# Performance work log

Measured on AMD Instinct MI355X. Metric: run time of the kernel, lower is better.

The kernel has to match this reference:

```python
import jax, jax.numpy as jnp
import numpy as np

HIDDEN = 256
HEADS = 1
HEAD_DIM = HIDDEN // HEADS  # internal_dim == hidden (downsample_rate=1)
SQ = 4096        # 64x64 current-frame tokens
N_MEM = 4        # memory frames
N_OBJ = 64       # object-pointer tokens excluded from RoPE
SK = N_MEM * SQ + N_OBJ  # 16448


def _rotate_pairwise(x):
    # [x0, x1, x2, x3, ...] -> [-x1, x0, -x3, x2, ...]
    s = x.shape
    x = x.reshape(s[:-1] + (s[-1] // 2, 2))
    return jnp.stack([-x[..., 1], x[..., 0]], axis=-1).reshape(s)


def setup_inputs() -> dict:
    key = jax.random.key(0)
    ks = jax.random.split(key, 16)
    d = {}
    d["query"] = jax.random.normal(ks[0], (1, 1, SQ, HIDDEN), jnp.float32)
    d["key"] = jax.random.normal(ks[1], (1, 1, SK, HIDDEN), jnp.float32)
    d["value"] = jax.random.normal(ks[2], (1, 1, SK, HIDDEN), jnp.float32)
    # rotary tables broadcast over (B*P, heads) like in the keras code
    d["cos"] = jax.random.uniform(ks[3], (1, 1, SQ, HEAD_DIM), jnp.float32, -1.0, 1.0)
    d["sin"] = jax.random.uniform(ks[4], (1, 1, SQ, HEAD_DIM), jnp.float32, -1.0, 1.0)
    w = 0.02
    d["q_w"] = jax.random.normal(ks[5], (HIDDEN, HIDDEN), jnp.float32) * w
    d["q_b"] = jnp.zeros((HIDDEN,), jnp.float32)
    d["k_w"] = jax.random.normal(ks[6], (HIDDEN, HIDDEN), jnp.float32) * w
    d["k_b"] = jnp.zeros((HIDDEN,), jnp.float32)
    d["v_w"] = jax.random.normal(ks[7], (HIDDEN, HIDDEN), jnp.float32) * w
    d["v_b"] = jnp.zeros((HIDDEN,), jnp.float32)
    d["o_w"] = jax.random.normal(ks[8], (HIDDEN, HIDDEN), jnp.float32) * w
    d["o_b"] = jnp.zeros((HIDDEN,), jnp.float32)
    d["num_k_exclude_rope"] = N_OBJ
    return d


def reference(query, key, value, cos, sin, q_w, q_b, k_w, k_b, v_w, v_b, o_w, o_b, num_k_exclude_rope):
    B, P, Sq, _ = query.shape
    Sk = key.shape[2]
    nex = int(num_k_exclude_rope)

    def heads(x):  # (B,P,S,internal) -> (B*P, H, S, hd)
        s = x.shape
        return x.reshape(s[0] * s[1], s[2], HEADS, HEAD_DIM).transpose(0, 2, 1, 3)

    q = heads(query @ q_w + q_b)
    k = heads(key @ k_w + k_b)
    v = heads(value @ v_w + v_b)

    # 2D rotary embedding (fp32 math, as in the original)
    qf = q.astype(jnp.float32)
    q_emb = (qf * cos + _rotate_pairwise(qf) * sin).astype(q.dtype)

    k_rot = k[:, :, :Sk - nex, :]
    k_pass = k[:, :, Sk - nex:, :] if nex > 0 else None
    if k_rot.shape[2] != Sq:  # rope_k_repeat=True path
        rf = k_rot.shape[2] // Sq
        cos_k = jnp.repeat(cos, rf, axis=2)
        sin_k = jnp.repeat(sin, rf, axis=2)
    else:
        cos_k, sin_k = cos, sin
    kf = k_rot.astype(jnp.float32)
    k_emb = (kf * cos_k + _rotate_pairwise(kf) * sin_k).astype(k.dtype)
    if k_pass is not None:
        k_emb = jnp.concatenate([k_emb, k_pass], axis=2)

    scaling = HEAD_DIM ** -0.5
    scores = jnp.einsum('bhqd,bhkd->bhqk', q_emb, k_emb) * scaling
    attn = jax.nn.softmax(scores, axis=-1)
    out = jnp.einsum('bhqk,bhkd->bhqd', attn, v)  # (B*P, H, Sq, hd)
    out = out.transpose(0, 2, 1, 3).reshape(B, P, Sq, HEADS * HEAD_DIM)
    return out @ o_w + o_b
```

## Files before the change

kernel.cpp:

```cpp
#include <hip/hip_runtime.h>
#include <stdint.h>

typedef _Float16 half_t;
typedef __attribute__((ext_vector_type(8))) _Float16 f16x8;
typedef __attribute__((ext_vector_type(4))) _Float16 f16x4;
typedef __attribute__((ext_vector_type(4))) float f32x4;

#define SQN 4096
#define SKN 16448
#define NROPE 16384
#define NSPLIT 12
#define NTILES 514
#define SCQ 0.090168441360f

#define GLD16(gp, lp) __builtin_amdgcn_global_load_lds( \
    (const __attribute__((address_space(1))) void*)(const void*)(gp), \
    (__attribute__((address_space(3))) void*)(void*)(lp), 16, 0, 0)

__global__ __launch_bounds__(256) void wt_kernel(const float* __restrict__ qw,
    const float* __restrict__ kw, const float* __restrict__ vw, const float* __restrict__ ow,
    half_t* __restrict__ wt)
{
    __shared__ float tile[64][65];
    int b = blockIdx.x;
    int mat = b >> 4, t4 = b & 15;
    int k0 = (t4 >> 2) << 6, n0 = (t4 & 3) << 6;
    const float* W = (mat == 0) ? qw : (mat == 1) ? kw : (mat == 2) ? vw : ow;
    half_t* WT = wt + mat * 65536;
    int t = threadIdx.x;
#pragma unroll
    for (int j = 0; j < 16; ++j) {
        int e = j * 256 + t;
        tile[e >> 6][e & 63] = W[(k0 + (e >> 6)) * 256 + n0 + (e & 63)];
    }
    __syncthreads();
#pragma unroll
    for (int j = 0; j < 16; ++j) {
        int e = j * 256 + t;
        WT[(n0 + (e >> 6)) * 256 + k0 + (e & 63)] = (half_t)tile[e & 63][e >> 6];
    }
}

__global__ __launch_bounds__(256) void proj_kernel(
    const float* __restrict__ query, const float* __restrict__ key, const float* __restrict__ value,
    const float* __restrict__ cosp, const float* __restrict__ sinp,
    const half_t* __restrict__ wt,
    const float* __restrict__ qb, const float* __restrict__ kb, const float* __restrict__ vb,
    half_t* __restrict__ Qe, half_t* __restrict__ Ke, half_t* __restrict__ VTb)
{
    __shared__ __align__(16) half_t S[64 * 264];

    int b = blockIdx.x;
    int mode; long row0;
    const float* X; const half_t* W; const float* bias;
    if (b < 64)       { mode = 0; row0 = (long)b * 64;         X = query; W = wt;           bias = qb; }
    else if (b < 321) { mode = 1; row0 = (long)(b - 64) * 64;  X = key;   W = wt + 65536;   bias = kb; }
    else              { mode = 2; row0 = (long)(b - 321) * 64; X = value; W = wt + 131072;  bias = vb; }

    int tid = threadIdx.x;
    int w = tid >> 6, l = tid & 63;
    int l16 = l & 15, l4 = l >> 4;
    long rw0 = row0 + w * 16;

    f32x4 acc[16];
#pragma unroll
    for (int i = 0; i < 16; ++i) acc[i] = (f32x4){0.f, 0.f, 0.f, 0.f};

    const float* xrow = X + (rw0 + l16) * 256;
    for (int ks = 0; ks < 8; ++ks) {
        f32x4 xa = *reinterpret_cast<const f32x4*>(xrow + ks * 32 + l4 * 8);
        f32x4 xb = *reinterpret_cast<const f32x4*>(xrow + ks * 32 + l4 * 8 + 4);
        f16x8 af;
#pragma unroll
        for (int j = 0; j < 4; ++j) { af[j] = (half_t)xa[j]; af[4 + j] = (half_t)xb[j]; }
#pragma unroll
        for (int nt = 0; nt < 16; ++nt) {
            f16x8 bf = *reinterpret_cast<const f16x8*>(W + (nt * 16 + l16) * 256 + ks * 32 + l4 * 8);
            acc[nt] = __builtin_amdgcn_mfma_f32_16x16x32_f16(af, bf, acc[nt], 0, 0, 0);
        }
    }

    bool dorope = (mode == 0) || (mode == 1 && row0 < NROPE);
#pragma unroll
    for (int nt = 0; nt < 16; ++nt) {
        int d = nt * 16 + l16;
        float bv = bias[d];
        f32x4 v = acc[nt];
#pragma unroll
        for (int r = 0; r < 4; ++r) v[r] += bv;
        if (dorope) {
#pragma unroll
            for (int r = 0; r < 4; ++r) {
                long m = rw0 + l4 * 4 + r;
                long crow = (mode == 0) ? m : (m >> 2);
                float c = cosp[crow * 256 + d];
                float s = sinp[crow * 256 + d];
                float val = v[r];
                float other = __shfl_xor(val, 1);
                float rot = (d & 1) ? other : -other;
                v[r] = val * c + rot * s;
                if (mode == 0) v[r] *= SCQ;
            }
        }
        if (mode == 2) {
            long kv = rw0 + l4 * 4;
            long kvb = kv >> 5;
            int  kvw = (int)(kv & 31);
            f16x4 pk;
#pragma unroll
            for (int r = 0; r < 4; ++r) pk[r] = (half_t)v[r];
            *reinterpret_cast<f16x4*>(VTb + kvb * 8192 + (long)d * 32 + kvw) = pk;
        } else {
            int wrow = w * 16 + l4 * 4;
#pragma unroll
            for (int r = 0; r < 4; ++r)
                S[(wrow + r) * 264 + d] = (half_t)v[r];
        }
    }

    if (mode != 2) {
        __syncthreads();
        half_t* O = ((mode == 0) ? Qe : Ke) + row0 * 256;
#pragma unroll
        for (int i = 0; i < 8; ++i) {
            int e = (i * 256 + tid) * 8;
            int row = e >> 8, col = e & 255;
            f16x8 val = *reinterpret_cast<const f16x8*>(&S[row * 264 + col]);
            *reinterpret_cast<f16x8*>(O + e) = val;
        }
    }
}

__global__ __launch_bounds__(256, 3) void flash_kernel(
    const half_t* __restrict__ Qe, const half_t* __restrict__ Ke, const half_t* __restrict__ VTb,
    half_t* __restrict__ AOp, float* __restrict__ Lse)
{
    __shared__ __align__(16) half_t Ks[32 * 256];
    __shared__ __align__(16) half_t Vs[256 * 32];
    __shared__ __align__(16) half_t Ps[4][16 * 40];

    int b = blockIdx.x;
    int qb = b & 63;
    int chunk = b >> 6;
    int tid = threadIdx.x;
    int w = tid >> 6, l = tid & 63;
    int l16 = l & 15, l4 = l >> 4;
    long qw0 = (long)qb * 64 + w * 16;

    int t0 = (NTILES * chunk) / NSPLIT;
    int t1 = (NTILES * (chunk + 1)) / NSPLIT;

    f16x8 qf[8];
#pragma unroll
    for (int ks = 0; ks < 8; ++ks)
        qf[ks] = *reinterpret_cast<const f16x8*>(Qe + (qw0 + l16) * 256 + ks * 32 + l4 * 8);

    f32x4 o[16];
#pragma unroll
    for (int i = 0; i < 16; ++i) o[i] = (f32x4){0.f, 0.f, 0.f, 0.f};
    float mrun = -3.0e38f;
    float lsum = 0.0f;

#define STAGE(t) do {                                                        \
        const half_t* kb_ = Ke + (long)(t) * 32 * 256;                       \
        const half_t* vb_ = VTb + (long)(t) * 8192;                          \
        _Pragma("unroll")                                                    \
        for (int j = 0; j < 4; ++j) {                                        \
            int pb = w * 4096 + j * 1024;                                    \
            int p  = pb + l * 16;                                            \
            int row = p >> 9;                                                \
            int cols = ((p >> 4) & 31) ^ (row & 7);                          \
            GLD16(kb_ + row * 256 + cols * 8, Ks + (pb >> 1));               \
            GLD16(vb_ + (p >> 1), Vs + (pb >> 1));                           \
        }                                                                    \
    } while (0)

    STAGE(t0);
    __syncthreads();

    half_t* Pw = Ps[w];
    const int xk = l16 & 7;

    for (int t = t0; t < t1; ++t) {
        f32x4 s0 = (f32x4){0.f, 0.f, 0.f, 0.f};
        f32x4 s1 = (f32x4){0.f, 0.f, 0.f, 0.f};
#pragma unroll
        for (int ks = 0; ks < 8; ++ks) {
            int slot = ((ks * 4 + l4) ^ xk) << 3;
            f16x8 ka0 = *reinterpret_cast<const f16x8*>(Ks + l16 * 256 + slot);
            f16x8 ka1 = *reinterpret_cast<const f16x8*>(Ks + (16 + l16) * 256 + slot);
            s0 = __builtin_amdgcn_mfma_f32_16x16x32_f16(ka0, qf[ks], s0, 0, 0, 0);
            s1 = __builtin_amdgcn_mfma_f32_16x16x32_f16(ka1, qf[ks], s1, 0, 0, 0);
        }

        float tv[8];
#pragma unroll
        for (int r = 0; r < 4; ++r) { tv[r] = s0[r]; tv[4 + r] = s1[r]; }
        float pm = tv[0];
#pragma unroll
        for (int i = 1; i < 8; ++i) pm = fmaxf(pm, tv[i]);
        pm = fmaxf(pm, __shfl_xor(pm, 16));
        pm = fmaxf(pm, __shfl_xor(pm, 32));

        if (!__all(pm - mrun <= 8.0f)) {
            float mn = fmaxf(mrun, pm);
            float alpha = __builtin_amdgcn_exp2f(mrun - mn);
            lsum *= alpha;
            float ao[4];
#pragma unroll
            for (int r = 0; r < 4; ++r) ao[r] = __shfl(alpha, l4 * 4 + r);
#pragma unroll
            for (int i = 0; i < 16; ++i)
#pragma unroll
                for (int r = 0; r < 4; ++r) o[i][r] *= ao[r];
            mrun = mn;
        }

        float p[8];
        float psum = 0.f;
#pragma unroll
        for (int i = 0; i < 8; ++i) { p[i] = __builtin_amdgcn_exp2f(tv[i] - mrun); psum += p[i]; }
        psum += __shfl_xor(psum, 16);
        psum += __shfl_xor(psum, 32);
        lsum += psum;

        f16x4 pk0, pk1;
#pragma unroll
        for (int r = 0; r < 4; ++r) { pk0[r] = (half_t)p[r]; pk1[r] = (half_t)p[4 + r]; }
        *reinterpret_cast<f16x4*>(Pw + l16 * 40 + l4 * 4) = pk0;
        *reinterpret_cast<f16x4*>(Pw + l16 * 40 + 16 + l4 * 4) = pk1;

        f16x8 pa = *reinterpret_cast<const f16x8*>(Pw + l16 * 40 + l4 * 8);
#pragma unroll
        for (int nt = 0; nt < 16; ++nt) {
            f16x8 vbf = *reinterpret_cast<const f16x8*>(Vs + (nt * 16 + l16) * 32 + l4 * 8);
            o[nt] = __builtin_amdgcn_mfma_f32_16x16x32_f16(pa, vbf, o[nt], 0, 0, 0);
        }

        if (t + 1 < t1) {
            __syncthreads();
            STAGE(t + 1);
            __syncthreads();
        }
    }
#undef STAGE

    float inv[4];
#pragma unroll
    for (int r = 0; r < 4; ++r) inv[r] = 1.0f / __shfl(lsum, l4 * 4 + r);
    half_t* Ab = AOp + ((long)chunk * SQN + qw0) * 256;
#pragma unroll
    for (int nt = 0; nt < 16; ++nt)
#pragma unroll
        for (int r = 0; r < 4; ++r)
            Ab[(l4 * 4 + r) * 256 + nt * 16 + l16] = (half_t)(o[nt][r] * inv[r]);
    if (l < 16)
        Lse[(long)chunk * SQN + qw0 + l16] = mrun + __builtin_amdgcn_logf(lsum);
}

__global__ __launch_bounds__(256) void reduce_kernel(
    const half_t* __restrict__ AOp, const float* __restrict__ Lse, half_t* __restrict__ AO)
{
    int tid = threadIdx.x;
    long q = (long)blockIdx.x * 4 + (tid >> 6);
    int d0 = (tid & 63) * 4;
    float ls[NSPLIT];
    float lmax = -3.0e38f;
#pragma unroll
    for (int i = 0; i < NSPLIT; ++i) { ls[i] = Lse[(long)i * SQN + q]; lmax = fmaxf(lmax, ls[i]); }
    f32x4 acc = (f32x4){0.f, 0.f, 0.f, 0.f};
    float wsum = 0.f;
#pragma unroll
    for (int i = 0; i < NSPLIT; ++i) {
        float wgt = __builtin_amdgcn_exp2f(ls[i] - lmax);
        wsum += wgt;
        f16x4 ov = *reinterpret_cast<const f16x4*>(AOp + ((long)i * SQN + q) * 256 + d0);
#pragma unroll
        for (int r = 0; r < 4; ++r) acc[r] += wgt * (float)ov[r];
    }
    float inv = 1.0f / wsum;
    f16x4 pk;
#pragma unroll
    for (int r = 0; r < 4; ++r) pk[r] = (half_t)(acc[r] * inv);
    *reinterpret_cast<f16x4*>(AO + q * 256 + d0) = pk;
}

__global__ __launch_bounds__(256) void oproj_kernel(
    const half_t* __restrict__ AO, const half_t* __restrict__ WTo,
    const float* __restrict__ ob, float* __restrict__ out)
{
    int b = blockIdx.x;
    int tid = threadIdx.x;
    int w = tid >> 6, l = tid & 63;
    int l16 = l & 15, l4 = l >> 4;
    long r0 = (long)b * 64 + w * 16;
    f32x4 acc[16];
#pragma unroll
    for (int i = 0; i < 16; ++i) acc[i] = (f32x4){0.f, 0.f, 0.f, 0.f};
#pragma unroll
    for (int ks = 0; ks < 8; ++ks) {
        f16x8 af = *reinterpret_cast<const f16x8*>(AO + (r0 + l16) * 256 + ks * 32 + l4 * 8);
#pragma unroll
        for (int nt = 0; nt < 16; ++nt) {
            f16x8 bf = *reinterpret_cast<const f16x8*>(WTo + (nt * 16 + l16) * 256 + ks * 32 + l4 * 8);
            acc[nt] = __builtin_amdgcn_mfma_f32_16x16x32_f16(af, bf, acc[nt], 0, 0, 0);
        }
    }
#pragma unroll
    for (int nt = 0; nt < 16; ++nt) {
        int d = nt * 16 + l16;
        float bv = ob[d];
#pragma unroll
        for (int r = 0; r < 4; ++r)
            out[(r0 + l4 * 4 + r) * 256 + d] = acc[nt][r] + bv;
    }
}

extern "C" void kernel_launch(void* const* d_in, const int* in_sizes, int n_in,
                              void* d_out, int out_size, void* d_ws, size_t ws_size,
                              hipStream_t stream) {
    const float* query = (const float*)d_in[0];
    const float* key   = (const float*)d_in[1];
    const float* value = (const float*)d_in[2];
    const float* cosp  = (const float*)d_in[3];
    const float* sinp  = (const float*)d_in[4];
    const float* qw = (const float*)d_in[5];
    const float* qb = (const float*)d_in[6];
    const float* kw = (const float*)d_in[7];
    const float* kb = (const float*)d_in[8];
    const float* vw = (const float*)d_in[9];
    const float* vb = (const float*)d_in[10];
    const float* ow = (const float*)d_in[11];
    const float* ob = (const float*)d_in[12];

    char* ws = (char*)d_ws;
    half_t* Qe  = (half_t*)(ws);
    half_t* Ke  = (half_t*)(ws + 2097152);
    half_t* VTb = (half_t*)(ws + 10518528);
    half_t* WT  = (half_t*)(ws + 18939904);
    half_t* AOp = (half_t*)(ws + 19464192);
    float*  Lse = (float*)(ws + 44630016);
    half_t* AO  = (half_t*)(ws + 44826624);

    hipLaunchKernelGGL(wt_kernel, dim3(64), dim3(256), 0, stream, qw, kw, vw, ow, WT);
    hipLaunchKernelGGL(proj_kernel, dim3(578), dim3(256), 0, stream,
                       query, key, value, cosp, sinp, WT, qb, kb, vb, Qe, Ke, VTb);
    hipLaunchKernelGGL(flash_kernel, dim3(64 * NSPLIT), dim3(256), 0, stream, Qe, Ke, VTb, AOp, Lse);
    hipLaunchKernelGGL(reduce_kernel, dim3(1024), dim3(256), 0, stream, AOp, Lse, AO);
    hipLaunchKernelGGL(oproj_kernel, dim3(64), dim3(256), 0, stream, AO, WT + 3 * 65536, ob, (float*)d_out);
}
```

Baseline: 205.3 us.

## Double-buffer flash K/V tiles, cut split count, fuse split-reduce into output projection

The flash kernel now double-buffers the K and V tiles in LDS. The next tile's global-to-LDS loads are issued before the current tile's compute, so each iteration waits on one barrier instead of two. The split count drops from 12 to 8 and the launch bound is lowered to 2 blocks per CU to fit the doubled LDS. The block index now interleaves chunks within each query block. The separate reduce kernel is removed and the log-sum-exp merge of partial outputs happens inside the output-projection kernel, which uses 16-row blocks for more parallelism and avoids writing and re-reading the merged attention output. The costs are lower occupancy and fewer splits for the flash kernel, and redundant partial-output reads across the four waves of each oproj block.

```diff
diff --git a/kernel.cpp b/kernel.cpp
--- a/kernel.cpp
+++ b/kernel.cpp
@@ -9,7 +9,7 @@
 #define SQN 4096
 #define SKN 16448
 #define NROPE 16384
-#define NSPLIT 12
+#define NSPLIT 8
 #define NTILES 514
 #define SCQ 0.090168441360f
 
@@ -131,17 +131,17 @@
     }
 }
 
-__global__ __launch_bounds__(256, 3) void flash_kernel(
+__global__ __launch_bounds__(256, 2) void flash_kernel(
     const half_t* __restrict__ Qe, const half_t* __restrict__ Ke, const half_t* __restrict__ VTb,
     half_t* __restrict__ AOp, float* __restrict__ Lse)
 {
-    __shared__ __align__(16) half_t Ks[32 * 256];
-    __shared__ __align__(16) half_t Vs[256 * 32];
+    __shared__ __align__(16) half_t Ks[2][32 * 256];
+    __shared__ __align__(16) half_t Vs[2][256 * 32];
     __shared__ __align__(16) half_t Ps[4][16 * 40];
 
     int b = blockIdx.x;
-    int qb = b & 63;
-    int chunk = b >> 6;
+    int chunk = b & 7;
+    int qb = b >> 3;
     int tid = threadIdx.x;
     int w = tid >> 6, l = tid & 63;
     int l16 = l & 15, l4 = l >> 4;
@@ -161,34 +161,43 @@
     float mrun = -3.0e38f;
     float lsum = 0.0f;
 
-#define STAGE(t) do {                                                        \
-        const half_t* kb_ = Ke + (long)(t) * 32 * 256;                       \
+#define STAGE(d_, t) do {                                                    \
+        const half_t* kb_ = Ke + (long)(t) * 8192;                           \
         const half_t* vb_ = VTb + (long)(t) * 8192;                          \
+        half_t* ksd = &Ks[d_][0];                                            \
+        half_t* vsd = &Vs[d_][0];                                            \
         _Pragma("unroll")                                                    \
         for (int j = 0; j < 4; ++j) {                                        \
             int pb = w * 4096 + j * 1024;                                    \
             int p  = pb + l * 16;                                            \
             int row = p >> 9;                                                \
             int cols = ((p >> 4) & 31) ^ (row & 7);                          \
-            GLD16(kb_ + row * 256 + cols * 8, Ks + (pb >> 1));               \
-            GLD16(vb_ + (p >> 1), Vs + (pb >> 1));                           \
+            GLD16(kb_ + row * 256 + cols * 8, ksd + (pb >> 1));              \
+            GLD16(vb_ + (p >> 1), vsd + (pb >> 1));                          \
         }                                                                    \
     } while (0)
 
-    STAGE(t0);
-    __syncthreads();
+    STAGE(0, t0);
+    asm volatile("s_waitcnt vmcnt(0)" ::: "memory");
+    __builtin_amdgcn_s_barrier();
 
     half_t* Pw = Ps[w];
     const int xk = l16 & 7;
+    int cur = 0;
 
     for (int t = t0; t < t1; ++t) {
+        if (t + 1 < t1) STAGE(cur ^ 1, t + 1);
+
+        const half_t* KsC = &Ks[0][0] + cur * (32 * 256);
+        const half_t* VsC = &Vs[0][0] + cur * (256 * 32);
+
         f32x4 s0 = (f32x4){0.f, 0.f, 0.f, 0.f};
         f32x4 s1 = (f32x4){0.f, 0.f, 0.f, 0.f};
 #pragma unroll
         for (int ks = 0; ks < 8; ++ks) {
             int slot = ((ks * 4 + l4) ^ xk) << 3;
-            f16x8 ka0 = *reinterpret_cast<const f16x8*>(Ks + l16 * 256 + slot);
-            f16x8 ka1 = *reinterpret_cast<const f16x8*>(Ks + (16 + l16) * 256 + slot);
+            f16x8 ka0 = *reinterpret_cast<const f16x8*>(KsC + l16 * 256 + slot);
+            f16x8 ka1 = *reinterpret_cast<const f16x8*>(KsC + (16 + l16) * 256 + slot);
             s0 = __builtin_amdgcn_mfma_f32_16x16x32_f16(ka0, qf[ks], s0, 0, 0, 0);
             s1 = __builtin_amdgcn_mfma_f32_16x16x32_f16(ka1, qf[ks], s1, 0, 0, 0);
         }
@@ -233,15 +242,13 @@
         f16x8 pa = *reinterpret_cast<const f16x8*>(Pw + l16 * 40 + l4 * 8);
 #pragma unroll
         for (int nt = 0; nt < 16; ++nt) {
-            f16x8 vbf = *reinterpret_cast<const f16x8*>(Vs + (nt * 16 + l16) * 32 + l4 * 8);
+            f16x8 vbf = *reinterpret_cast<const f16x8*>(VsC + (nt * 16 + l16) * 32 + l4 * 8);
             o[nt] = __builtin_amdgcn_mfma_f32_16x16x32_f16(pa, vbf, o[nt], 0, 0, 0);
         }
 
-        if (t + 1 < t1) {
-            __syncthreads();
-            STAGE(t + 1);
-            __syncthreads();
-        }
+        asm volatile("s_waitcnt vmcnt(0)" ::: "memory");
+        __builtin_amdgcn_s_barrier();
+        cur ^= 1;
     }
 #undef STAGE
 
@@ -258,57 +265,60 @@
         Lse[(long)chunk * SQN + qw0 + l16] = mrun + __builtin_amdgcn_logf(lsum);
 }
 
-__global__ __launch_bounds__(256) void reduce_kernel(
-    const half_t* __restrict__ AOp, const float* __restrict__ Lse, half_t* __restrict__ AO)
-{
-    int tid = threadIdx.x;
-    long q = (long)blockIdx.x * 4 + (tid >> 6);
-    int d0 = (tid & 63) * 4;
-    float ls[NSPLIT];
-    float lmax = -3.0e38f;
-#pragma unroll
-    for (int i = 0; i < NSPLIT; ++i) { ls[i] = Lse[(long)i * SQN + q]; lmax = fmaxf(lmax, ls[i]); }
-    f32x4 acc = (f32x4){0.f, 0.f, 0.f, 0.f};
-    float wsum = 0.f;
-#pragma unroll
-    for (int i = 0; i < NSPLIT; ++i) {
-        float wgt = __builtin_amdgcn_exp2f(ls[i] - lmax);
-        wsum += wgt;
-        f16x4 ov = *reinterpret_cast<const f16x4*>(AOp + ((long)i * SQN + q) * 256 + d0);
-#pragma unroll
-        for (int r = 0; r < 4; ++r) acc[r] += wgt * (float)ov[r];
-    }
-    float inv = 1.0f / wsum;
-    f16x4 pk;
-#pragma unroll
-    for (int r = 0; r < 4; ++r) pk[r] = (half_t)(acc[r] * inv);
-    *reinterpret_cast<f16x4*>(AO + q * 256 + d0) = pk;
-}
-
 __global__ __launch_bounds__(256) void oproj_kernel(
-    const half_t* __restrict__ AO, const half_t* __restrict__ WTo,
-    const float* __restrict__ ob, float* __restrict__ out)
+    const half_t* __restrict__ AOp, const float* __restrict__ Lse,
+    const half_t* __restrict__ WTo, const float* __restrict__ ob,
+    float* __restrict__ out)
 {
     int b = blockIdx.x;
     int tid = threadIdx.x;
     int w = tid >> 6, l = tid & 63;
     int l16 = l & 15, l4 = l >> 4;
-    long r0 = (long)b * 64 + w * 16;
-    f32x4 acc[16];
-#pragma unroll
-    for (int i = 0; i < 16; ++i) acc[i] = (f32x4){0.f, 0.f, 0.f, 0.f};
+    long row = (long)b * 16 + l16;
+
+    float ls[NSPLIT];
+    float lmax = -3.0e38f;
+#pragma unroll
+    for (int c = 0; c < NSPLIT; ++c) { ls[c] = Lse[(long)c * SQN + row]; lmax = fmaxf(lmax, ls[c]); }
+    float wgt[NSPLIT];
+    float wsum = 0.f;
+#pragma unroll
+    for (int c = 0; c < NSPLIT; ++c) { wgt[c] = __builtin_amdgcn_exp2f(ls[c] - lmax); wsum += wgt[c]; }
+    float invw = 1.0f / wsum;
+#pragma unroll
+    for (int c = 0; c < NSPLIT; ++c) wgt[c] *= invw;
+
+    f32x4 acc[4];
+#pragma unroll
+    for (int i = 0; i < 4; ++i) acc[i] = (f32x4){0.f, 0.f, 0.f, 0.f};
+
 #pragma unroll
     for (int ks = 0; ks < 8; ++ks) {
-        f16x8 af = *reinterpret_cast<const f16x8*>(AO + (r0 + l16) * 256 + ks * 32 + l4 * 8);
-#pragma unroll
-        for (int nt = 0; nt < 16; ++nt) {
-            f16x8 bf = *reinterpret_cast<const f16x8*>(WTo + (nt * 16 + l16) * 256 + ks * 32 + l4 * 8);
+        float facc[8];
+#pragma unroll
+        for (int j = 0; j < 8; ++j) facc[j] = 0.f;
+#pragma unroll
+        for (int c = 0; c < NSPLIT; ++c) {
+            f16x8 v = *reinterpret_cast<const f16x8*>(
+                AOp + ((long)c * SQN + row) * 256 + ks * 32 + l4 * 8);
+#pragma unroll
+            for (int j = 0; j < 8; ++j) facc[j] += wgt[c] * (float)v[j];
+        }
+        f16x8 af;
+#pragma unroll
+        for (int j = 0; j < 8; ++j) af[j] = (half_t)facc[j];
+#pragma unroll
+        for (int nt = 0; nt < 4; ++nt) {
+            f16x8 bf = *reinterpret_cast<const f16x8*>(
+                WTo + ((w * 4 + nt) * 16 + l16) * 256 + ks * 32 + l4 * 8);
             acc[nt] = __builtin_amdgcn_mfma_f32_16x16x32_f16(af, bf, acc[nt], 0, 0, 0);
         }
     }
-#pragma unroll
-    for (int nt = 0; nt < 16; ++nt) {
-        int d = nt * 16 + l16;
+
+    long r0 = (long)b * 16;
+#pragma unroll
+    for (int nt = 0; nt < 4; ++nt) {
+        int d = (w * 4 + nt) * 16 + l16;
         float bv = ob[d];
 #pragma unroll
         for (int r = 0; r < 4; ++r)
@@ -339,13 +349,11 @@
     half_t* VTb = (half_t*)(ws + 10518528);
     half_t* WT  = (half_t*)(ws + 18939904);
     half_t* AOp = (half_t*)(ws + 19464192);
-    float*  Lse = (float*)(ws + 44630016);
-    half_t* AO  = (half_t*)(ws + 44826624);
+    float*  Lse = (float*)(ws + 36241408);
 
     hipLaunchKernelGGL(wt_kernel, dim3(64), dim3(256), 0, stream, qw, kw, vw, ow, WT);
     hipLaunchKernelGGL(proj_kernel, dim3(578), dim3(256), 0, stream,
                        query, key, value, cosp, sinp, WT, qb, kb, vb, Qe, Ke, VTb);
-    hipLaunchKernelGGL(flash_kernel, dim3(64 * NSPLIT), dim3(256), 0, stream, Qe, Ke, VTb, AOp, Lse);
-    hipLaunchKernelGGL(reduce_kernel, dim3(1024), dim3(256), 0, stream, AOp, Lse, AO);
-    hipLaunchKernelGGL(oproj_kernel, dim3(64), dim3(256), 0, stream, AO, WT + 3 * 65536, ob, (float*)d_out);
-}
+    hipLaunchKernelGGL(flash_kernel, dim3(512), dim3(256), 0, stream, Qe, Ke, VTb, AOp, Lse);
+    hipLaunchKernelGGL(oproj_kernel, dim3(256), dim3(256), 0, stream, AOp, Lse, WT + 3 * 65536, ob, (float*)d_out);
+}
```

After: 188.4 us. -8.2%, faster.
